# Performance work log

Measured on AMD Instinct MI355X. Metric: run time of the kernel, lower is better.

Reference implementation:

```python
import jax, jax.numpy as jnp
import numpy as np

N_PTS, HID, N_LAYERS, N_HEAD, B = 21, 128, 4, 4, 8192
EPS_LN = 1e-6


def _cheb(x, adj, W, b):
    # ChebConv with K=2 (3 orders): T0=I, T1=L, T2=2*L@L - I, L = I - D^-1/2 A D^-1/2
    d = jnp.sum(adj, axis=-1) ** -0.5
    L = jnp.eye(N_PTS, dtype=x.dtype) - d[:, None] * adj * d[None, :]
    t1 = jnp.einsum('ij,bjc->bic', L, x)
    t2 = 2.0 * jnp.einsum('ij,bjc->bic', L, t1) - x
    return (jnp.einsum('bnc,cd->bnd', x, W[0])
            + jnp.einsum('bnc,cd->bnd', t1, W[1])
            + jnp.einsum('bnc,cd->bnd', t2, W[2])) + b


def _layer_norm(x, a, b):
    # matches custom LayerNorm: unbiased std (torch default), eps added to std
    mean = jnp.mean(x, -1, keepdims=True)
    xm = x - mean
    std = jnp.sqrt(jnp.sum(xm * xm, -1, keepdims=True) / (x.shape[-1] - 1))
    return a * xm / (std + EPS_LN) + b


def _mha(x, mask, Wq, bq, Wk, bk, Wv, bv, Wo, bo):
    Bn, N, D = x.shape
    dk = D // N_HEAD
    def proj(W, b):
        return (x @ W + b).reshape(Bn, N, N_HEAD, dk).transpose(0, 2, 1, 3)
    Q, K, V = proj(Wq, bq), proj(Wk, bk), proj(Wv, bv)
    scores = jnp.einsum('bhqd,bhkd->bhqk', Q, K) / np.float32(np.sqrt(dk))
    scores = jnp.where(mask[:, None, :, :], scores, jnp.asarray(-1e9, x.dtype))
    p = jax.nn.softmax(scores, axis=-1)  # dropout is identity at eval
    o = jnp.einsum('bhqk,bhkd->bhqd', p, V).transpose(0, 2, 1, 3).reshape(Bn, N, D)
    return o @ Wo + bo


def _graphnet(x, Ahat, W1, b1, W2, b2):
    # GraphNet feed-forward: two GraphConvs with learnable A_hat
    # laplacian_batch: D from column sums (torch.sum over dim=1), A_hat same per batch
    d = (jnp.sum(Ahat, axis=0) + 1e-5) ** -0.5
    L = d[:, None] * Ahat * d[None, :]
    h = jax.nn.relu(jnp.einsum('ij,bjc->bic', L, x) @ W1 + b1)
    return jnp.einsum('ij,bjc->bic', L, h) @ W2 + b2


def _forward(x, mask, adj, W_in, b_in, W_out, b_out, ln1_a, ln1_b, ln2_a, ln2_b,
             Wq, bq, Wk, bk, Wv, bv, Wo, bo, Ahat, Wg1, bg1, Wg2, bg2,
             Wc1, bc1, Wc2, bc2):
    out = _cheb(x, adj, W_in, b_in)  # [B,21,128]
    for i in range(N_LAYERS):
        # EncoderLayer: pre-norm residual attn, then pre-norm residual GraphNet
        h = _layer_norm(out, ln1_a[i], ln1_b[i])
        out = out + _mha(h, mask, Wq[i], bq[i], Wk[i], bk[i], Wv[i], bv[i], Wo[i], bo[i])
        h = _layer_norm(out, ln2_a[i], ln2_b[i])
        out = out + _graphnet(h, Ahat[i], Wg1[i], bg1[i], Wg2[i], bg2[i])
        # _ResChebGC: residual + relu(cheb(relu(cheb(x))))
        g = jax.nn.relu(_cheb(out, adj, Wc1[i], bc1[i]))
        out = out + jax.nn.relu(_cheb(g, adj, Wc2[i], bc2[i]))
    return _cheb(out, adj, W_out, b_out)  # [B,21,3]


def setup_inputs() -> dict:
    key = jax.random.key(0)
    ks = iter(jax.random.split(key, 40))
    def nrm(shape, s=0.02):
        return jax.random.normal(next(ks), shape, jnp.float32) * s
    L = N_LAYERS
    return dict(
        x=jax.random.normal(next(ks), (B, N_PTS, 2), jnp.float32),
        mask=jnp.ones((1, 1, N_PTS), dtype=bool),
        adj=jax.random.uniform(next(ks), (N_PTS, N_PTS), jnp.float32) + jnp.eye(N_PTS, dtype=jnp.float32),
        W_in=nrm((3, 2, HID), 0.2), b_in=jnp.zeros((HID,), jnp.float32),
        W_out=nrm((3, HID, 3), 0.05), b_out=jnp.zeros((3,), jnp.float32),
        ln1_a=jnp.ones((L, HID), jnp.float32), ln1_b=jnp.zeros((L, HID), jnp.float32),
        ln2_a=jnp.ones((L, HID), jnp.float32), ln2_b=jnp.zeros((L, HID), jnp.float32),
        Wq=nrm((L, HID, HID)), bq=jnp.zeros((L, HID), jnp.float32),
        Wk=nrm((L, HID, HID)), bk=jnp.zeros((L, HID), jnp.float32),
        Wv=nrm((L, HID, HID)), bv=jnp.zeros((L, HID), jnp.float32),
        Wo=nrm((L, HID, HID)), bo=jnp.zeros((L, HID), jnp.float32),
        Ahat=jnp.tile(jnp.eye(N_PTS, dtype=jnp.float32)[None], (L, 1, 1)),
        Wg1=nrm((L, HID, 2 * HID)), bg1=jnp.zeros((L, 2 * HID), jnp.float32),
        Wg2=nrm((L, 2 * HID, HID)), bg2=jnp.zeros((L, HID), jnp.float32),
        Wc1=nrm((L, 3, HID, HID)), bc1=jnp.zeros((L, HID), jnp.float32),
        Wc2=nrm((L, 3, HID, HID)), bc2=jnp.zeros((L, HID), jnp.float32),
    )


def reference(x, mask, adj, W_in, b_in, W_out, b_out, ln1_a, ln1_b, ln2_a, ln2_b,
              Wq, bq, Wk, bk, Wv, bv, Wo, bo, Ahat, Wg1, bg1, Wg2, bg2,
              Wc1, bc1, Wc2, bc2):
    return _forward(x, mask, adj, W_in, b_in, W_out, b_out, ln1_a, ln1_b, ln2_a, ln2_b,
                    Wq, bq, Wk, bk, Wv, bv, Wo, bo, Ahat, Wg1, bg1, Wg2, bg2,
                    Wc1, bc1, Wc2, bc2)
```

## Files before the change

### kernel.cpp

```cpp
#include <hip/hip_runtime.h>

#define DEV static __device__ __forceinline__

typedef __attribute__((ext_vector_type(8))) short short8;
typedef __attribute__((ext_vector_type(4))) short short4v;
typedef __attribute__((ext_vector_type(4))) float f4;

#define OFF_QKV 0
#define OFF_WO  196608
#define OFF_WG1 262144
#define OFF_WG2 393216
#define OFF_WC1 524288
#define OFF_WC2 720896
#define OFF_WIN 917504
#define OFF_WOUT 929792
#define OFF_M1 931840
#define OFF_M2 932864
#define OFF_LG 933888
#define W_TOT  937984

struct WSBuf {
  unsigned short w[W_TOT];
  float m1f[441];
  float m2f[441];
};
__device__ WSBuf g_ws;

DEV float b2f(unsigned short u){ union { unsigned int i; float f; } v; v.i = ((unsigned int)u)<<16; return v.f; }
DEV unsigned short f2b(float f){
  union { float f; unsigned int i; } v; v.f = f;
  unsigned int i = v.i; i += 0x7fffu + ((i>>16)&1u);
  return (unsigned short)(i>>16);
}
DEV f4 mfma(short8 a, short8 b, f4 c){ return __builtin_amdgcn_mfma_f32_16x16x32_bf16(a,b,c,0,0,0); }
DEV f4 mfma16(short4v a, short4v b, f4 c){ return __builtin_amdgcn_mfma_f32_16x16x16bf16_1k(a,b,c,0,0,0); }
DEV short8 ld8(const unsigned short* p){ return *(const short8*)p; }

DEV void st4(unsigned short* p, f4 v){
  short4v o;
  o[0]=(short)f2b(v[0]); o[1]=(short)f2b(v[1]);
  o[2]=(short)f2b(v[2]); o[3]=(short)f2b(v[3]);
  *(short4v*)p = o;
}
DEV void rmw4(unsigned short* p, f4 v){
  short4v x = *(const short4v*)p;
  short4v o;
  o[0]=(short)f2b(b2f((unsigned short)x[0]) + v[0]);
  o[1]=(short)f2b(b2f((unsigned short)x[1]) + v[1]);
  o[2]=(short)f2b(b2f((unsigned short)x[2]) + v[2]);
  o[3]=(short)f2b(b2f((unsigned short)x[3]) + v[3]);
  *(short4v*)p = o;
}
DEV f4 maxz(f4 v){
  v[0]=fmaxf(v[0],0.f); v[1]=fmaxf(v[1],0.f);
  v[2]=fmaxf(v[2],0.f); v[3]=fmaxf(v[3],0.f);
  return v;
}

__global__ void prep_mats(const float* __restrict__ adj,
                          const float* __restrict__ Ahat){
  __shared__ float sA[441], sL[441], sM2[441], sD[21];
  unsigned short* ws = g_ws.w;
  int t = threadIdx.x;
  if (t < 441) sA[t] = adj[t];
  __syncthreads();
  if (t < 21){ float s = 0.f; for (int j=0;j<21;++j) s += sA[t*21+j]; sD[t] = 1.0f/sqrtf(s); }
  __syncthreads();
  if (t < 441){ int i = t/21, j = t%21; sL[t] = ((i==j)?1.f:0.f) - sD[i]*sA[t]*sD[j]; }
  __syncthreads();
  if (t < 441){ int i = t/21, j = t%21; float a=0.f;
    for (int m=0;m<21;++m) a += sL[i*21+m]*sL[m*21+j];
    sM2[t] = 2.f*a - ((i==j)?1.f:0.f); }
  __syncthreads();
  for (int e = t; e < 1024; e += blockDim.x){
    int i = e>>5, j = e&31; bool v = (i<21)&&(j<21);
    ws[OFF_M1+e] = v ? f2b(sL[i*21+j]) : 0;
    ws[OFF_M2+e] = v ? f2b(sM2[i*21+j]) : 0;
  }
  if (t < 441){ g_ws.m1f[t] = sL[t]; g_ws.m2f[t] = sM2[t]; }
  for (int l=0;l<4;++l){
    __syncthreads();
    if (t < 441) sA[t] = Ahat[l*441 + t];
    __syncthreads();
    if (t < 21){ float s = 1e-5f; for (int i=0;i<21;++i) s += sA[i*21+t]; sD[t] = 1.0f/sqrtf(s); }
    __syncthreads();
    for (int e = t; e < 1024; e += blockDim.x){
      int i = e>>5, j = e&31; bool v = (i<21)&&(j<21);
      ws[OFF_LG + l*1024 + e] = v ? f2b(sD[i]*sA[i*21+j]*sD[j]) : 0;
    }
  }
}

__global__ void prep_tw(const float* __restrict__ Wq, const float* __restrict__ Wk,
                        const float* __restrict__ Wv, const float* __restrict__ Wo,
                        const float* __restrict__ Wg1, const float* __restrict__ Wg2,
                        const float* __restrict__ Wc1, const float* __restrict__ Wc2,
                        const float* __restrict__ Win, const float* __restrict__ Wout){
  unsigned short* ws = g_ws.w;
  int stride = gridDim.x*blockDim.x;
  int idx = blockIdx.x*blockDim.x + threadIdx.x;
  for (int e = idx; e < 196608; e += stride){
    int l = e/49152, r = e%49152, n = r>>7, k = r&127;
    int sel = n>>7, c = n&127;
    const float* W = (sel==0)?Wq:((sel==1)?Wk:Wv);
    ws[OFF_QKV+e] = f2b(W[l*16384 + k*128 + c]);
  }
  for (int e = idx; e < 65536; e += stride){
    int l = e>>14, r = e&16383, n = r>>7, k = r&127;
    ws[OFF_WO+e] = f2b(Wo[l*16384 + k*128 + n]);
  }
  for (int e = idx; e < 131072; e += stride){
    int l = e>>15, r = e&32767, n = r>>7, k = r&127;
    ws[OFF_WG1+e] = f2b(Wg1[l*32768 + k*256 + n]);
  }
  for (int e = idx; e < 131072; e += stride){
    int l = e>>15, r = e&32767, n = r>>8, k = r&255;
    ws[OFF_WG2+e] = f2b(Wg2[l*32768 + k*128 + n]);
  }
  for (int e = idx; e < 196608; e += stride){
    int l = e/49152, r = e%49152, n = r>>7, k = r&127;
    int sel = n>>7, c = n&127;
    ws[OFF_WC1+e] = f2b(Wc1[((l*3+sel)*128 + k)*128 + c]);
  }
  for (int e = idx; e < 196608; e += stride){
    int l = e/49152, r = e%49152, n = r>>7, k = r&127;
    int sel = n>>7, c = n&127;
    ws[OFF_WC2+e] = f2b(Wc2[((l*3+sel)*128 + k)*128 + c]);
  }
  for (int e = idx; e < 12288; e += stride){
    int n = e>>5, k = e&31, sel = n>>7, c = n&127;
    ws[OFF_WIN+e] = (k<2) ? f2b(Win[(sel*2 + k)*128 + c]) : 0;
  }
  for (int e = idx; e < 2048; e += stride){
    int n = e>>7, k = e&127;
    ws[OFF_WOUT+e] = (n<9) ? f2b(Wout[((n/3)*128 + k)*3 + (n%3)]) : 0;
  }
}

#define PA 152

template<int MT, int NT, int KS>
DEV void chan_mm(const unsigned short* A, int pitchA,
                 const unsigned short* Bt, int strideB, int n0, int mt0,
                 int lane, f4 acc[MT][NT]){
  const int l16 = lane & 15, qd = lane >> 4;
#pragma unroll
  for (int ks = 0; ks < KS; ++ks){
    const int k0 = ks*32 + qd*8;
    short8 af[MT];
#pragma unroll
    for (int m=0; m<MT; ++m) af[m] = ld8(A + ((mt0+m)*16+l16)*pitchA + k0);
#pragma unroll
    for (int nt=0; nt<NT; ++nt){
      short8 bf = ld8(Bt + (n0 + nt*16 + l16)*strideB + k0);
#pragma unroll
      for (int m=0; m<MT; ++m) acc[m][nt] = mfma(af[m], bf, acc[m][nt]);
    }
  }
}

DEV void node_mm1(const unsigned short* Ut, int mt0,
                  const unsigned short* Mr, int lane, f4 acc[3][2]){
  const int l16 = lane & 15, qd = lane >> 4;
  short8 bf[2];
#pragma unroll
  for (int nt=0; nt<2; ++nt) bf[nt] = ld8(Mr + (nt*16+l16)*32 + qd*8);
#pragma unroll
  for (int b=0;b<3;++b){
    short8 af = ld8(Ut + (mt0*16 + l16)*72 + b*24 + qd*8);
#pragma unroll
    for (int nt=0;nt<2;++nt) acc[b][nt] = mfma(af, bf[nt], acc[b][nt]);
  }
}

template<int KS>
DEV void w0_term1(const unsigned short* Wt0, int sK,
                  const unsigned short* Blds, int pitchB, int mt0,
                  int lane, f4 acc[3][2]){
  const int l16 = lane&15, qd = lane>>4;
#pragma unroll
  for (int ks=0; ks<KS; ++ks){
    const int k0 = ks*32 + qd*8;
    short8 af = ld8(Wt0 + (mt0*16+l16)*sK + k0);
#pragma unroll
    for (int b=0;b<3;++b){
#pragma unroll
      for (int nt=0;nt<2;++nt){
        short8 bf = ld8(Blds + (b*21 + nt*16 + l16)*pitchB + k0);
        acc[b][nt] = mfma(af, bf, acc[b][nt]);
      }
    }
  }
}

DEV void write_tr(unsigned short* Ut, int ch, f4 v, int mt, int qd, float bias, int rmax){
#pragma unroll
  for (int reg=0; reg<4; ++reg){
    int r = mt*16 + qd*4 + reg;
    if (r < rmax){
      int b = (r>=42) ? 2 : ((r>=21)?1:0);
      int n = r - b*21;
      Ut[ch*72 + b*24 + n] = f2b(v[reg] + bias);
    }
  }
}

DEV void layer_norm(const unsigned short* src, unsigned short* dst,
                    const float* ga, const float* gb, int tid){
  int row = tid >> 3, seg = tid & 7;
  const unsigned short* p = src + row*136 + seg*16;
  float xv[16];
#pragma unroll
  for (int j=0;j<2;++j){
    short8 rv = ld8(p + j*8);
#pragma unroll
    for (int i=0;i<8;++i) xv[j*8+i] = b2f((unsigned short)rv[i]);
  }
  float s1=0.f, s2=0.f;
#pragma unroll
  for (int i=0;i<16;++i){ s1 += xv[i]; s2 += xv[i]*xv[i]; }
  s1 += __shfl_xor(s1,1); s2 += __shfl_xor(s2,1);
  s1 += __shfl_xor(s1,2); s2 += __shfl_xor(s2,2);
  s1 += __shfl_xor(s1,4); s2 += __shfl_xor(s2,4);
  float mean = s1 * 0.0078125f;
  float var = (s2 - s1*mean) * (1.0f/127.0f);
  var = fmaxf(var, 0.f);
  float inv = 1.0f/(sqrtf(var) + 1e-6f);
  unsigned short* d = dst + row*PA + seg*16;
#pragma unroll
  for (int j=0;j<2;++j){
    short8 ov;
#pragma unroll
    for (int i=0;i<8;++i){
      float y = ga[seg*16+j*8+i] * (xv[j*8+i]-mean) * inv + gb[seg*16+j*8+i];
      ov[i] = (short)f2b(y);
    }
    *(short8*)(d + j*8) = ov;
  }
}

#define R_RES 0
#define R_A   8704
#define R_TR  18432
#define TRU   9232
#define S_TOT 37368

DEV void cheb_res(const unsigned short* Asrc, int pitchA,
                  const unsigned short* Wcat, const float* bias,
                  bool writeG,
                  unsigned short* s_a, unsigned short* s_tr, unsigned short* s_res,
                  const unsigned short* M1r, const unsigned short* M2r,
                  int lane, int wave, int nb, int rvalid){
  const int l16 = lane&15, qd = lane>>4;
  const f4 z4 = {0.f,0.f,0.f,0.f};
#pragma unroll
  for (int p=1; p<=2; ++p){
    f4 acc[4][1];
#pragma unroll
    for (int mt=0;mt<4;++mt) acc[mt][0]=z4;
    chan_mm<4,1,4>(Asrc, pitchA, Wcat, 128, p*128 + wave*16, 0, lane, acc);
    unsigned short* Ut = (p==1) ? s_tr : (s_tr + TRU);
    int ch = wave*16 + l16;
#pragma unroll
    for (int mt=0;mt<4;++mt) write_tr(Ut, ch, acc[mt][0], mt, qd, 0.f, rvalid);
  }
  f4 a2[3][2];
#pragma unroll
  for (int b=0;b<3;++b){ a2[b][0]=z4; a2[b][1]=z4; }
  w0_term1<4>(Wcat, 128, Asrc, pitchA, wave, lane, a2);
  node_mm1(s_tr, wave, M1r, lane, a2);
  node_mm1(s_tr + TRU, wave, M2r, lane, a2);
  const int ch0 = wave*16 + qd*4;
  const f4 vb = *(const f4*)(bias + ch0);
#pragma unroll
  for (int b=0;b<3;++b){ if (b >= nb) continue;
#pragma unroll
    for (int nt=0;nt<2;++nt){
      int o = nt*16 + l16;
      if (o < 21){
        int r = b*21 + o;
        f4 t = maxz(a2[b][nt] + vb);
        if (writeG) st4(&s_a[r*PA + ch0], t);
        else        rmw4(&s_res[r*136 + ch0], t);
      }
    }
  }
  __syncthreads();
}

__launch_bounds__(512, 1)
__global__ void graformer_main(
  const float* __restrict__ x,
  const float* __restrict__ ln1a, const float* __restrict__ ln1b,
  const float* __restrict__ ln2a, const float* __restrict__ ln2b,
  const float* __restrict__ bq, const float* __restrict__ bk,
  const float* __restrict__ bv, const float* __restrict__ bo,
  const float* __restrict__ bg1, const float* __restrict__ bg2,
  const float* __restrict__ bc1, const float* __restrict__ bc2,
  const float* __restrict__ b_in, const float* __restrict__ b_out,
  float* __restrict__ out)
{
  __shared__ __align__(16) unsigned short S[S_TOT];
  unsigned short* s_res = S + R_RES;
  unsigned short* s_a   = S + R_A;
  unsigned short* s_tr  = S + R_TR;
  const unsigned short* ws = g_ws.w;

  const int tid = threadIdx.x;
  const int lane = tid & 63, wave = tid >> 6;
  const int l16 = lane & 15, qd = lane >> 4;
  const int blk = blockIdx.x;
  int nb = 8192 - blk*3; nb = (nb < 3) ? nb : 3;
  const int rvalid = nb*21;
  const f4 z4 = {0.f,0.f,0.f,0.f};
  const unsigned short* M1r = ws + OFF_M1;
  const unsigned short* M2r = ws + OFF_M2;
  const int mh2 = (wave>>2)*2, nq = (wave&3)*32;
  const int ch0 = wave*16 + qd*4;

  {
    short8 z8 = {0,0,0,0,0,0,0,0};
    for (int i = tid*8; i < S_TOT; i += 512*8) *(short8*)(S + i) = z8;
  }
  __syncthreads();

  if (tid < 64){
    int r = tid;
    float v0=0.f, v1=0.f;
    if (r < rvalid){
      int b = (r>=42)?2:((r>=21)?1:0);
      int n = r - b*21;
      long g = (long)(blk*3+b)*42 + n*2;
      v0 = x[g]; v1 = x[g+1];
    }
    unsigned short* p = s_a + r*32;
    p[0]=f2b(v0); p[1]=f2b(v1);
#pragma unroll
    for (int k=2;k<32;++k) p[k]=0;
  }
  __syncthreads();

  {
#pragma unroll
    for (int p=1; p<=2; ++p){
      f4 acc[4][1];
#pragma unroll
      for (int mt=0;mt<4;++mt) acc[mt][0]=z4;
      chan_mm<4,1,1>(s_a, 32, ws + OFF_WIN, 32, p*128 + wave*16, 0, lane, acc);
      unsigned short* Ut = (p==1) ? s_tr : (s_tr + TRU);
      int ch = wave*16 + l16;
#pragma unroll
      for (int mt=0;mt<4;++mt) write_tr(Ut, ch, acc[mt][0], mt, qd, 0.f, rvalid);
    }
    f4 a2[3][2];
#pragma unroll
    for (int b=0;b<3;++b){ a2[b][0]=z4; a2[b][1]=z4; }
    w0_term1<1>(ws + OFF_WIN, 32, s_a, 32, wave, lane, a2);
    node_mm1(s_tr, wave, M1r, lane, a2);
    node_mm1(s_tr + TRU, wave, M2r, lane, a2);
    const f4 vbin = *(const f4*)(b_in + ch0);
#pragma unroll
    for (int b=0;b<3;++b){ if (b>=nb) continue;
#pragma unroll
      for (int nt=0;nt<2;++nt){
        int o = nt*16 + l16;
        if (o < 21){ int r = b*21 + o;
          st4(&s_res[r*136 + ch0], a2[b][nt] + vbin);
        }
      }
    }
    __syncthreads();
  }

  for (int l=0; l<4; ++l){
    layer_norm(s_res, s_a, ln1a + l*128, ln1b + l*128, tid);
    __syncthreads();
    {
      {
        f4 ak[1][4];
#pragma unroll
        for (int nt=0;nt<4;++nt) ak[0][nt]=z4;
        chan_mm<1,4,4>(ws + OFF_QKV + l*49152 + 16384, 128, s_a, PA, 0, wave, lane, ak);
        const f4 vbk = *(const f4*)(bk + l*128 + ch0);
#pragma unroll
        for (int nt=0;nt<4;++nt){
          int node = nt*16 + l16;
          st4(&s_tr[node*136 + ch0], ak[0][nt] + vbk);
        }
      }
      {
        f4 av[2][2]; av[0][0]=z4; av[0][1]=z4; av[1][0]=z4; av[1][1]=z4;
        chan_mm<2,2,4>(s_a, PA, ws + OFF_QKV + l*49152 + 32768, 128, nq, mh2, lane, av);
#pragma unroll
        for (int nt=0;nt<2;++nt){
          int ch = nq + nt*16 + l16; float bb = bv[l*128+ch];
#pragma unroll
          for (int m=0;m<2;++m) write_tr(s_tr+8704, ch, av[m][nt], mh2+m, qd, bb, rvalid);
        }
      }
      f4 aq[1][4];
#pragma unroll
      for (int nt=0;nt<4;++nt) aq[0][nt]=z4;
      chan_mm<1,4,4>(ws + OFF_QKV + l*49152, 128, s_a, PA, 0, wave, lane, aq);
      __syncthreads();
      {
        const f4 vbq = *(const f4*)(bq + l*128 + ch0);
#pragma unroll
        for (int nt=0;nt<4;++nt){
          int node = nt*16 + l16;
          st4(&s_a[node*PA + ch0], aq[0][nt] + vbq);
        }
      }
      __syncthreads();
    }
    {
#pragma unroll
      for (int i=0;i<3;++i){
        int u = wave + 8*i;
        int pair = u >> 1, mt = u & 1;
        int b = pair>>2, h = pair&3;
        f4 sc[2]; sc[0]=z4; sc[1]=z4;
        short8 qb = ld8(s_a + (b*21 + mt*16 + l16)*PA + h*32 + qd*8);
#pragma unroll
        for (int nt=0;nt<2;++nt){
          short8 ka = ld8(s_tr + (b*21 + nt*16 + l16)*136 + h*32 + qd*8);
          sc[nt] = mfma(ka, qb, sc[nt]);
        }
        const float scale = 0.1767766952966369f;
        float s0[4], s1[4];
        float m = -1e30f;
#pragma unroll
        for (int reg=0;reg<4;++reg){
          s0[reg] = sc[0][reg]*scale;
          bool kv = (16 + qd*4 + reg) < 21;
          s1[reg] = kv ? sc[1][reg]*scale : -1e30f;
          m = fmaxf(m, fmaxf(s0[reg], s1[reg]));
        }
        m = fmaxf(m, __shfl_xor(m,16));
        m = fmaxf(m, __shfl_xor(m,32));
        float e0[4], e1[4];
        float sum = 0.f;
#pragma unroll
        for (int reg=0;reg<4;++reg){
          e0[reg] = __expf(s0[reg]-m);
          e1[reg] = ((16+qd*4+reg)<21) ? __expf(s1[reg]-m) : 0.f;
          sum += e0[reg]+e1[reg];
        }
        sum += __shfl_xor(sum,16);
        sum += __shfl_xor(sum,32);
        float rinv = 1.f/sum;
        if (b < nb){
          short4v pa0, pa1;
#pragma unroll
          for (int reg=0;reg<4;++reg){
            pa0[reg] = (short)f2b(e0[reg]*rinv);
            pa1[reg] = (short)f2b(e1[reg]*rinv);
          }
          f4 oa[2]; oa[0]=z4; oa[1]=z4;
#pragma unroll
          for (int nt=0;nt<2;++nt){
            int ch = h*32 + nt*16 + l16;
            const unsigned short* vp = s_tr + 8704 + ch*72 + b*24;
            short4v vb0 = *(const short4v*)(vp + qd*4);
            short4v vb1 = *(const short4v*)(vp + 16 + qd*4);
            oa[nt] = mfma16(pa0, vb0, oa[nt]);
            oa[nt] = mfma16(pa1, vb1, oa[nt]);
          }
#pragma unroll
          for (int reg=0;reg<4;++reg){
            int qn = mt*16+qd*4+reg;
            if (qn < 21){
#pragma unroll
              for (int nt=0;nt<2;++nt)
                s_a[(b*21+qn)*PA + h*32 + nt*16 + l16] = f2b(oa[nt][reg]);
            }
          }
        }
      }
      __syncthreads();
    }
    {
      f4 ao[1][4];
#pragma unroll
      for (int nt=0;nt<4;++nt) ao[0][nt]=z4;
      chan_mm<1,4,4>(ws + OFF_WO + l*16384, 128, s_a, PA, 0, wave, lane, ao);
      const f4 vbo = *(const f4*)(bo + l*128 + ch0);
#pragma unroll
      for (int nt=0;nt<4;++nt){
        int node = nt*16 + l16;
        if (node < rvalid)
          rmw4(&s_res[node*136 + ch0], ao[0][nt] + vbo);
      }
      __syncthreads();
    }
    layer_norm(s_res, s_a, ln2a + l*128, ln2b + l*128, tid);
    __syncthreads();
    {
      {
        f4 u[4][1];
#pragma unroll
        for (int mt=0;mt<4;++mt) u[mt][0]=z4;
        chan_mm<4,1,4>(s_a, PA, ws + OFF_WG1 + l*32768, 128, wave*16, 0, lane, u);
        int ch = wave*16 + l16;
#pragma unroll
        for (int mt=0;mt<4;++mt) write_tr(s_tr, ch, u[mt][0], mt, qd, 0.f, rvalid);
        f4 y[3][2];
#pragma unroll
        for (int b=0;b<3;++b){ y[b][0]=z4; y[b][1]=z4; }
        node_mm1(s_tr, wave, ws + OFF_LG + l*1024, lane, y);
        const f4 vb1 = *(const f4*)(bg1 + l*256 + ch0);
#pragma unroll
        for (int b=0;b<3;++b){ if (b>=nb) continue;
#pragma unroll
          for (int nt=0;nt<2;++nt){
            int o = nt*16+l16;
            if (o<21){ int r = b*21+o;
              st4(&s_tr[TRU + r*PA + ch0], maxz(y[b][nt] + vb1));
            }
          }
        }
      }
      {
        f4 u[4][1];
#pragma unroll
        for (int mt=0;mt<4;++mt) u[mt][0]=z4;
        chan_mm<4,1,4>(s_a, PA, ws + OFF_WG1 + l*32768 + 16384, 128, wave*16, 0, lane, u);
        int ch = wave*16 + l16;
#pragma unroll
        for (int mt=0;mt<4;++mt) write_tr(s_tr, ch, u[mt][0], mt, qd, 0.f, rvalid);
      }
      __syncthreads();
      {
        f4 y[3][2];
#pragma unroll
        for (int b=0;b<3;++b){ y[b][0]=z4; y[b][1]=z4; }
        node_mm1(s_tr, wave, ws + OFF_LG + l*1024, lane, y);
        const f4 vb1b = *(const f4*)(bg1 + l*256 + 128 + ch0);
#pragma unroll
        for (int b=0;b<3;++b){ if (b>=nb) continue;
#pragma unroll
          for (int nt=0;nt<2;++nt){
            int o = nt*16+l16;
            if (o<21){ int r = b*21+o;
              st4(&s_a[r*PA + ch0], maxz(y[b][nt] + vb1b));
            }
          }
        }
      }
      __syncthreads();
      f4 Z[4][1];
#pragma unroll
      for (int mt=0;mt<4;++mt) Z[mt][0]=z4;
      chan_mm<4,1,4>(s_tr + TRU, PA, ws + OFF_WG2 + l*32768, 256, wave*16, 0, lane, Z);
      chan_mm<4,1,4>(s_a, PA, ws + OFF_WG2 + l*32768 + 128, 256, wave*16, 0, lane, Z);
      __syncthreads();
      {
        int ch = wave*16 + l16;
#pragma unroll
        for (int mt=0;mt<4;++mt) write_tr(s_a, ch, Z[mt][0], mt, qd, 0.f, rvalid);
      }
      f4 fz[3][2];
#pragma unroll
      for (int b=0;b<3;++b){ fz[b][0]=z4; fz[b][1]=z4; }
      node_mm1(s_a, wave, ws + OFF_LG + l*1024, lane, fz);
      {
        const f4 vb2 = *(const f4*)(bg2 + l*128 + ch0);
#pragma unroll
        for (int b=0;b<3;++b){ if (b>=nb) continue;
#pragma unroll
          for (int nt=0;nt<2;++nt){
            int o = nt*16+l16;
            if (o<21){ int r = b*21+o;
              rmw4(&s_res[r*136 + ch0], fz[b][nt] + vb2);
            }
          }
        }
      }
      __syncthreads();
    }
    cheb_res(s_res, 136, ws + OFF_WC1 + l*49152, bc1 + l*128, true,
             s_a, s_tr, s_res, M1r, M2r, lane, wave, nb, rvalid);
    cheb_res(s_a, PA, ws + OFF_WC2 + l*49152, bc2 + l*128, false,
             s_a, s_tr, s_res, M1r, M2r, lane, wave, nb, rvalid);
  }

  {
    f4 acc = z4;
    if (wave < 4){
#pragma unroll
      for (int ks=0;ks<4;++ks){
        int k0 = ks*32 + qd*8;
        short8 af = ld8(s_res + (wave*16 + l16)*136 + k0);
        short8 bf = ld8(ws + OFF_WOUT + l16*128 + k0);
        acc = mfma(af, bf, acc);
      }
    }
    float* sf = (float*)s_a;
    if (wave < 4 && l16 < 9){
#pragma unroll
      for (int reg=0;reg<4;++reg){
        int r = wave*16 + qd*4 + reg;
        if (r < 63) sf[r*12 + l16] = acc[reg];
      }
    }
    __syncthreads();
    if (tid < 189){
      int r = tid/3, c = tid - r*3;
      int b = (r>=42)?2:((r>=21)?1:0);
      int n = r - b*21;
      if (b < nb){
        const float* M1f = g_ws.m1f;
        const float* M2f = g_ws.m2f;
        float a = sf[r*12 + c] + b_out[c];
        for (int m=0;m<21;++m){
          a += M1f[n*21+m]*sf[(b*21+m)*12 + 3 + c];
          a += M2f[n*21+m]*sf[(b*21+m)*12 + 6 + c];
        }
        out[((long)(blk*3+b)*21 + n)*3 + c] = a;
      }
    }
  }
}

extern "C" void kernel_launch(void* const* d_in, const int* in_sizes, int n_in,
                              void* d_out, int out_size, void* d_ws, size_t ws_size,
                              hipStream_t stream){
  const float* x    = (const float*)d_in[0];
  const float* adj  = (const float*)d_in[2];
  const float* Win  = (const float*)d_in[3];
  const float* b_in = (const float*)d_in[4];
  const float* Wout = (const float*)d_in[5];
  const float* b_out= (const float*)d_in[6];
  const float* ln1a = (const float*)d_in[7];
  const float* ln1b = (const float*)d_in[8];
  const float* ln2a = (const float*)d_in[9];
  const float* ln2b = (const float*)d_in[10];
  const float* Wq = (const float*)d_in[11];
  const float* bq = (const float*)d_in[12];
  const float* Wk = (const float*)d_in[13];
  const float* bk = (const float*)d_in[14];
  const float* Wv = (const float*)d_in[15];
  const float* bv = (const float*)d_in[16];
  const float* Wo = (const float*)d_in[17];
  const float* bo = (const float*)d_in[18];
  const float* Ahat = (const float*)d_in[19];
  const float* Wg1 = (const float*)d_in[20];
  const float* bg1 = (const float*)d_in[21];
  const float* Wg2 = (const float*)d_in[22];
  const float* bg2 = (const float*)d_in[23];
  const float* Wc1 = (const float*)d_in[24];
  const float* bc1 = (const float*)d_in[25];
  const float* Wc2 = (const float*)d_in[26];
  const float* bc2 = (const float*)d_in[27];
  float* outp = (float*)d_out;

  hipLaunchKernelGGL(prep_mats, dim3(1), dim3(512), 0, stream, adj, Ahat);
  hipLaunchKernelGGL(prep_tw, dim3(512), dim3(256), 0, stream,
                     Wq, Wk, Wv, Wo, Wg1, Wg2, Wc1, Wc2, Win, Wout);
  hipLaunchKernelGGL(graformer_main, dim3(2731), dim3(512), 0, stream,
                     x, ln1a, ln1b, ln2a, ln2b, bq, bk, bv, bo,
                     bg1, bg2, bc1, bc2, b_in, b_out, outp);
}
```

Before: 1.381 ms.

## Add dedicated LDS buffers for Q and GraphNet hidden to drop barriers

Q projections and the first GraphNet hidden activations now go into new shared-memory regions instead of reusing s_a. This lets several __syncthreads be removed, since writes no longer overwrite data other waves may still be reading. The attention P·V MFMA operands are also swapped so each lane holds four consecutive channels, allowing vectorized 4-wide stores in place of scalar ones. The cost is a larger LDS footprint and correctness that now depends on per-wave channel ownership in the write_tr/node_mm1 pairs.

```diff
diff --git a/kernel.cpp b/kernel.cpp
--- a/kernel.cpp
+++ b/kernel.cpp
@@ -243,7 +243,9 @@
 #define R_A   8704
 #define R_TR  18432
 #define TRU   9232
-#define S_TOT 37368
+#define R_Q   37368
+#define R_Y1  47096
+#define S_TOT 56824
 
 DEV void cheb_res(const unsigned short* Asrc, int pitchA,
                   const unsigned short* Wcat, const float* bias,
@@ -304,6 +306,8 @@
   unsigned short* s_res = S + R_RES;
   unsigned short* s_a   = S + R_A;
   unsigned short* s_tr  = S + R_TR;
+  unsigned short* s_q   = S + R_Q;
+  unsigned short* s_y1  = S + R_Y1;
   const unsigned short* ws = g_ws.w;
 
   const int tid = threadIdx.x;
@@ -315,7 +319,6 @@
   const f4 z4 = {0.f,0.f,0.f,0.f};
   const unsigned short* M1r = ws + OFF_M1;
   const unsigned short* M2r = ws + OFF_M2;
-  const int mh2 = (wave>>2)*2, nq = (wave&3)*32;
   const int ch0 = wave*16 + qd*4;
 
   {
@@ -390,6 +393,7 @@
       }
       {
         f4 av[2][2]; av[0][0]=z4; av[0][1]=z4; av[1][0]=z4; av[1][1]=z4;
+        const int mh2 = (wave>>2)*2, nq = (wave&3)*32;
         chan_mm<2,2,4>(s_a, PA, ws + OFF_QKV + l*49152 + 32768, 128, nq, mh2, lane, av);
 #pragma unroll
         for (int nt=0;nt<2;++nt){
@@ -398,17 +402,16 @@
           for (int m=0;m<2;++m) write_tr(s_tr+8704, ch, av[m][nt], mh2+m, qd, bb, rvalid);
         }
       }
-      f4 aq[1][4];
-#pragma unroll
-      for (int nt=0;nt<4;++nt) aq[0][nt]=z4;
-      chan_mm<1,4,4>(ws + OFF_QKV + l*49152, 128, s_a, PA, 0, wave, lane, aq);
-      __syncthreads();
       {
+        f4 aq[1][4];
+#pragma unroll
+        for (int nt=0;nt<4;++nt) aq[0][nt]=z4;
+        chan_mm<1,4,4>(ws + OFF_QKV + l*49152, 128, s_a, PA, 0, wave, lane, aq);
         const f4 vbq = *(const f4*)(bq + l*128 + ch0);
 #pragma unroll
         for (int nt=0;nt<4;++nt){
           int node = nt*16 + l16;
-          st4(&s_a[node*PA + ch0], aq[0][nt] + vbq);
+          st4(&s_q[node*PA + ch0], aq[0][nt] + vbq);
         }
       }
       __syncthreads();
@@ -420,7 +423,7 @@
         int pair = u >> 1, mt = u & 1;
         int b = pair>>2, h = pair&3;
         f4 sc[2]; sc[0]=z4; sc[1]=z4;
-        short8 qb = ld8(s_a + (b*21 + mt*16 + l16)*PA + h*32 + qd*8);
+        short8 qb = ld8(s_q + (b*21 + mt*16 + l16)*PA + h*32 + qd*8);
 #pragma unroll
         for (int nt=0;nt<2;++nt){
           short8 ka = ld8(s_tr + (b*21 + nt*16 + l16)*136 + h*32 + qd*8);
@@ -463,17 +466,15 @@
             const unsigned short* vp = s_tr + 8704 + ch*72 + b*24;
             short4v vb0 = *(const short4v*)(vp + qd*4);
             short4v vb1 = *(const short4v*)(vp + 16 + qd*4);
-            oa[nt] = mfma16(pa0, vb0, oa[nt]);
-            oa[nt] = mfma16(pa1, vb1, oa[nt]);
+            oa[nt] = mfma16(vb0, pa0, oa[nt]);
+            oa[nt] = mfma16(vb1, pa1, oa[nt]);
           }
-#pragma unroll
-          for (int reg=0;reg<4;++reg){
-            int qn = mt*16+qd*4+reg;
-            if (qn < 21){
-#pragma unroll
-              for (int nt=0;nt<2;++nt)
-                s_a[(b*21+qn)*PA + h*32 + nt*16 + l16] = f2b(oa[nt][reg]);
-            }
+          int q = mt*16 + l16;
+          if (q < 21){
+            int row = (b*21 + q)*PA + h*32;
+#pragma unroll
+            for (int nt=0;nt<2;++nt)
+              st4(&s_a[row + nt*16 + qd*4], oa[nt]);
           }
         }
       }
@@ -528,9 +529,6 @@
         int ch = wave*16 + l16;
 #pragma unroll
         for (int mt=0;mt<4;++mt) write_tr(s_tr, ch, u[mt][0], mt, qd, 0.f, rvalid);
-      }
-      __syncthreads();
-      {
         f4 y[3][2];
 #pragma unroll
         for (int b=0;b<3;++b){ y[b][0]=z4; y[b][1]=z4; }
@@ -542,7 +540,7 @@
           for (int nt=0;nt<2;++nt){
             int o = nt*16+l16;
             if (o<21){ int r = b*21+o;
-              st4(&s_a[r*PA + ch0], maxz(y[b][nt] + vb1b));
+              st4(&s_y1[r*PA + ch0], maxz(y[b][nt] + vb1b));
             }
           }
         }
@@ -552,17 +550,16 @@
 #pragma unroll
       for (int mt=0;mt<4;++mt) Z[mt][0]=z4;
       chan_mm<4,1,4>(s_tr + TRU, PA, ws + OFF_WG2 + l*32768, 256, wave*16, 0, lane, Z);
-      chan_mm<4,1,4>(s_a, PA, ws + OFF_WG2 + l*32768 + 128, 256, wave*16, 0, lane, Z);
-      __syncthreads();
+      chan_mm<4,1,4>(s_y1, PA, ws + OFF_WG2 + l*32768 + 128, 256, wave*16, 0, lane, Z);
       {
         int ch = wave*16 + l16;
 #pragma unroll
-        for (int mt=0;mt<4;++mt) write_tr(s_a, ch, Z[mt][0], mt, qd, 0.f, rvalid);
+        for (int mt=0;mt<4;++mt) write_tr(s_tr, ch, Z[mt][0], mt, qd, 0.f, rvalid);
       }
       f4 fz[3][2];
 #pragma unroll
       for (int b=0;b<3;++b){ fz[b][0]=z4; fz[b][1]=z4; }
-      node_mm1(s_a, wave, ws + OFF_LG + l*1024, lane, fz);
+      node_mm1(s_tr, wave, ws + OFF_LG + l*1024, lane, fz);
       {
         const f4 vb2 = *(const f4*)(bg2 + l*128 + ch0);
 #pragma unroll
```

After: 1.356 ms. No clear change (-1.8%).
